# Optimization experiments

Measured on AMD Instinct MI355X. Metric: run time of the kernel, lower is better.

The kernel has to match this reference:

```python
import jax, jax.numpy as jnp
import numpy as np

TEMPERATURE = 0.05


def setup_inputs() -> dict:
    key = jax.random.key(0)
    k1, k2 = jax.random.split(key)
    B, D = 4096, 1024
    # scale 0.1 keeps pairwise distances O(3) so the original exp(-d/T) is sane
    text_embeddings = 0.1 * jax.random.normal(k1, (B, D), dtype=jnp.float32)
    image_embeddings = 0.1 * jax.random.normal(k2, (B, D), dtype=jnp.float32)
    positive_pairs = jnp.arange(B, dtype=jnp.int32)  # unused by the loss body
    return {
        "text_embeddings": text_embeddings,
        "image_embeddings": image_embeddings,
        "positive_pairs": positive_pairs,
    }


def _pairwise_l2(t, m):
    # ||t_i - m_j|| via GEMM expansion; [B, B]
    sq = (
        jnp.sum(t * t, axis=1, keepdims=True)
        + jnp.sum(m * m, axis=1)[None, :]
        - 2.0 * (t @ m.T)
    )
    return jnp.sqrt(jnp.maximum(sq, 0.0))


def reference(text_embeddings, image_embeddings, positive_pairs):
    # loss_i = -log( exp(-d_ii/T) / sum_{j != i} exp(-d_ij/T) )
    #        = logsumexp_{j != i}(-d_ij/T) + d_ii/T   (exact same math, stable)
    dist = _pairwise_l2(text_embeddings, image_embeddings)  # [B, B]
    logits = -dist / TEMPERATURE
    diag = jnp.diagonal(logits)  # log numerator per row
    B = logits.shape[0]
    eye = jnp.eye(B, dtype=bool)
    masked = jnp.where(eye, -jnp.inf, logits)  # exclude self-term from denom
    lse = jax.nn.logsumexp(masked, axis=1)
    return jnp.mean(lse - diag)
```

## Files before the change

kernel.cpp:

```cpp
#include <hip/hip_runtime.h>
#include <math.h>


#define NB 4096
#define ND 1024
#define LSE_BIAS 90.0f
#define A2 28.85390082f
#define C2 129.8425537f
#define LN2 0.6931471805599453f
#define SCALE1 0x7F7F7F7Fu

typedef int v8i __attribute__((ext_vector_type(8)));
typedef int int4v __attribute__((ext_vector_type(4)));
typedef float v16f __attribute__((ext_vector_type(16)));

__device__ inline void gload_lds16(const unsigned char* g, unsigned char* l) {
  __builtin_amdgcn_global_load_lds(
      (const __attribute__((address_space(1))) unsigned int*)g,
      (__attribute__((address_space(3))) unsigned int*)l, 16, 0, 0);
}

__global__ void prep_kernel(const float* __restrict__ T, const float* __restrict__ M,
                            unsigned char* __restrict__ t8, unsigned char* __restrict__ m8,
                            float* __restrict__ tn, float* __restrict__ mn,
                            float* __restrict__ out) {
  int row = blockIdx.x;
  if (row == 0 && threadIdx.x == 0) out[0] = 0.0f;
  const float* src;
  unsigned char* dst;
  float* nout;
  int r;
  if (row < NB) { src = T; dst = t8; nout = tn; r = row; }
  else          { src = M; dst = m8; nout = mn; r = row - NB; }
  float4 v = ((const float4*)(src + (size_t)r * ND))[threadIdx.x];
  float s = v.x * v.x + v.y * v.y + v.z * v.z + v.w * v.w;
  int p = __builtin_amdgcn_cvt_pk_fp8_f32(v.x, v.y, 0, false);
  p = __builtin_amdgcn_cvt_pk_fp8_f32(v.z, v.w, p, true);
  ((int*)(dst + (size_t)r * ND))[threadIdx.x] = p;
  for (int off = 32; off; off >>= 1) s += __shfl_xor(s, off);
  __shared__ float wsum[4];
  if ((threadIdx.x & 63) == 0) wsum[threadIdx.x >> 6] = s;
  __syncthreads();
  if (threadIdx.x == 0) nout[r] = wsum[0] + wsum[1] + wsum[2] + wsum[3];
}

__launch_bounds__(256, 3)
__global__ void gemm_lse_kernel(const unsigned char* __restrict__ t8,
                                const unsigned char* __restrict__ m8,
                                const float* __restrict__ tn, const float* __restrict__ mn,
                                float* __restrict__ part_s, float* __restrict__ diag) {
  __shared__ unsigned char Al[128 * 128];
  __shared__ unsigned char Bl[128 * 128];
  int rt = blockIdx.x, ct = blockIdx.y;
  int tid = threadIdx.x;
  int wave = tid >> 6, lane = tid & 63;
  int hb = lane >> 5, l31 = lane & 31;

  v16f acc[2][2] = {};

  int l3 = lane >> 3;
  int gc = (lane & 7) ^ l3;
  const unsigned char* gA = t8 + (size_t)(rt * 128 + wave * 32 + l3) * ND + gc * 16;
  const unsigned char* gB = m8 + (size_t)(ct * 128 + wave * 32 + l3) * ND + gc * 16;
  unsigned char* lA = Al + wave * 4096;
  unsigned char* lB = Bl + wave * 4096;

  int wr0 = (wave >> 1) * 64, wc0 = (wave & 1) * 64;
  int sw = l31 & 7;
  int abase = (wr0 + l31) * 128;
  int bbase = (wc0 + l31) * 128;

#pragma unroll 1
  for (int kt = 0; kt < ND / 128; ++kt) {
#pragma unroll
    for (int i = 0; i < 4; ++i) {
      gload_lds16(gA + (size_t)i * 8 * ND, lA + i * 1024);
      gload_lds16(gB + (size_t)i * 8 * ND, lB + i * 1024);
    }
    __syncthreads();
#pragma unroll
    for (int ks = 0; ks < 2; ++ks) {
      int q16 = ((ks * 4 + 2 * hb) ^ sw) * 16;
      int4v a00 = *(const int4v*)&Al[abase + q16];
      int4v a01 = *(const int4v*)&Al[abase + (q16 ^ 16)];
      int4v a10 = *(const int4v*)&Al[abase + 4096 + q16];
      int4v a11 = *(const int4v*)&Al[abase + 4096 + (q16 ^ 16)];
      v8i af0 = (v8i){a00.x, a00.y, a00.z, a00.w, a01.x, a01.y, a01.z, a01.w};
      v8i af1 = (v8i){a10.x, a10.y, a10.z, a10.w, a11.x, a11.y, a11.z, a11.w};
#pragma unroll
      for (int fc = 0; fc < 2; ++fc) {
        int4v b0 = *(const int4v*)&Bl[bbase + fc * 4096 + q16];
        int4v b1 = *(const int4v*)&Bl[bbase + fc * 4096 + (q16 ^ 16)];
        v8i bf = (v8i){b0.x, b0.y, b0.z, b0.w, b1.x, b1.y, b1.z, b1.w};
        acc[0][fc] = __builtin_amdgcn_mfma_scale_f32_32x32x64_f8f6f4(
            af0, bf, acc[0][fc], 0, 0, 0, SCALE1, 0, SCALE1);
        acc[1][fc] = __builtin_amdgcn_mfma_scale_f32_32x32x64_f8f6f4(
            af1, bf, acc[1][fc], 0, 0, 0, SCALE1, 0, SCALE1);
      }
    }
    __syncthreads();
    gA += 128;
    gB += 128;
  }

  int chunk = ct * 2 + (wave & 1);
  bool diagblk = (rt == ct);
  float mnv[2];
#pragma unroll
  for (int fc = 0; fc < 2; ++fc) mnv[fc] = mn[ct * 128 + wc0 + fc * 32 + l31];
#pragma unroll
  for (int fr = 0; fr < 2; ++fr) {
#pragma unroll
    for (int reg = 0; reg < 16; ++reg) {
      int row = (reg & 3) + 8 * (reg >> 2) + 4 * hb;
      int grow = rt * 128 + wr0 + fr * 32 + row;
      float tnr = tn[grow];
      float s = 0.0f;
#pragma unroll
      for (int fc = 0; fc < 2; ++fc) {
        float sq = fmaxf(fmaf(-2.0f, acc[fr][fc][reg], tnr + mnv[fc]), 0.0f);
        float dr = __builtin_amdgcn_sqrtf(sq);
        float e = __builtin_amdgcn_exp2f(fmaf(dr, -A2, C2));
        if (diagblk) {
          int gcol = ct * 128 + wc0 + fc * 32 + l31;
          if (grow == gcol) {
            diag[grow] = -20.0f * dr;
            e = 0.0f;
          }
        }
        s += e;
      }
      for (int m = 16; m; m >>= 1) s += __shfl_xor(s, m);
      if (l31 == 0) part_s[(size_t)grow * 64 + chunk] = s;
    }
  }
}

__global__ void combine_kernel(const float* __restrict__ part_s,
                               const float* __restrict__ diag, float* __restrict__ out) {
  int row = blockIdx.x * 256 + threadIdx.x;
  const float* ps = part_s + (size_t)row * 64;
  float S = 0.0f;
#pragma unroll 8
  for (int c = 0; c < 64; ++c) S += ps[c];
  float loss = (LN2 * __builtin_amdgcn_logf(S) - LSE_BIAS) - diag[row];
  for (int off = 32; off; off >>= 1) loss += __shfl_xor(loss, off);
  __shared__ float wsum[4];
  if ((threadIdx.x & 63) == 0) wsum[threadIdx.x >> 6] = loss;
  __syncthreads();
  if (threadIdx.x == 0)
    atomicAdd(out, (wsum[0] + wsum[1] + wsum[2] + wsum[3]) * (1.0f / (float)NB));
}

extern "C" void kernel_launch(void* const* d_in, const int* in_sizes, int n_in,
                              void* d_out, int out_size, void* d_ws, size_t ws_size,
                              hipStream_t stream) {
  const float* T = (const float*)d_in[0];
  const float* M = (const float*)d_in[1];
  float* out = (float*)d_out;

  unsigned char* t8 = (unsigned char*)d_ws;
  unsigned char* m8 = t8 + (size_t)NB * ND;
  float* fbase = (float*)(m8 + (size_t)NB * ND);
  float* tn = fbase;
  float* mn = tn + NB;
  float* diag = mn + NB;
  float* part_s = diag + NB;

  prep_kernel<<<2 * NB, 256, 0, stream>>>(T, M, t8, m8, tn, mn, out);
  dim3 grid(NB / 128, NB / 128);
  gemm_lse_kernel<<<grid, 256, 0, stream>>>(t8, m8, tn, mn, part_s, diag);
  combine_kernel<<<NB / 256, 256, 0, stream>>>(part_s, diag, out);
}
```

Measured before the change: 107.5 us.

## Use 256x256 tiles with double-buffered LDS staging and grouped block order

The fused GEMM+LSE kernel now computes a 256x256 output tile per 512-thread block instead of 128x128 per 256-thread block. Each wave now holds four row fragments, which raises operand reuse per LDS read. The kernel ping-pongs two LDS buffers, issuing the next K-slice's global-to-LDS loads before computing the current slice so load latency overlaps the MFMAs. It also remaps block indices into grouped regions for L2 locality and raises wave priority around the MFMA section. The cost is 128KB of LDS per block and more accumulator registers, so only one block fits per CU, and the 256-block grid roughly matches the CU count.

```diff
diff --git a/kernel.cpp b/kernel.cpp
--- a/kernel.cpp
+++ b/kernel.cpp
@@ -44,76 +44,92 @@
   if (threadIdx.x == 0) nout[r] = wsum[0] + wsum[1] + wsum[2] + wsum[3];
 }
 
-__launch_bounds__(256, 3)
+__launch_bounds__(512, 2)
 __global__ void gemm_lse_kernel(const unsigned char* __restrict__ t8,
                                 const unsigned char* __restrict__ m8,
                                 const float* __restrict__ tn, const float* __restrict__ mn,
                                 float* __restrict__ part_s, float* __restrict__ diag) {
-  __shared__ unsigned char Al[128 * 128];
-  __shared__ unsigned char Bl[128 * 128];
-  int rt = blockIdx.x, ct = blockIdx.y;
+  __shared__ unsigned char A0[256 * 128];
+  __shared__ unsigned char A1[256 * 128];
+  __shared__ unsigned char B0[256 * 128];
+  __shared__ unsigned char B1[256 * 128];
+  int b = blockIdx.x;
+  int region = b & 7, idx = b >> 3;
+  int rt = ((region >> 2) << 3) | (idx & 7);
+  int ct = ((region & 3) << 2) | (idx >> 3);
   int tid = threadIdx.x;
   int wave = tid >> 6, lane = tid & 63;
   int hb = lane >> 5, l31 = lane & 31;
+  int wr = wave >> 2, wc = wave & 3;
 
-  v16f acc[2][2] = {};
+  v16f acc[4][2] = {};
 
   int l3 = lane >> 3;
   int gc = (lane & 7) ^ l3;
-  const unsigned char* gA = t8 + (size_t)(rt * 128 + wave * 32 + l3) * ND + gc * 16;
-  const unsigned char* gB = m8 + (size_t)(ct * 128 + wave * 32 + l3) * ND + gc * 16;
-  unsigned char* lA = Al + wave * 4096;
-  unsigned char* lB = Bl + wave * 4096;
+  const unsigned char* gA = t8 + (size_t)(rt * 256 + wave * 32 + l3) * ND + gc * 16;
+  const unsigned char* gB = m8 + (size_t)(ct * 256 + wave * 32 + l3) * ND + gc * 16;
 
-  int wr0 = (wave >> 1) * 64, wc0 = (wave & 1) * 64;
   int sw = l31 & 7;
-  int abase = (wr0 + l31) * 128;
-  int bbase = (wc0 + l31) * 128;
+  int arow = (wr * 128 + l31) * 128;
+  int brow = (wc * 64 + l31) * 128;
+
+#define STAGE(DA, DB, koff)                                                  \
+  do {                                                                       \
+    _Pragma("unroll") for (int i = 0; i < 4; ++i) {                          \
+      gload_lds16(gA + (koff) + (size_t)i * 8 * ND, DA + wave * 4096 + i * 1024); \
+      gload_lds16(gB + (koff) + (size_t)i * 8 * ND, DB + wave * 4096 + i * 1024); \
+    }                                                                        \
+  } while (0)
+
+#define COMPUTE(SA, SB)                                                      \
+  do {                                                                       \
+    _Pragma("unroll") for (int ks = 0; ks < 2; ++ks) {                       \
+      int q16 = ((ks * 4 + 2 * hb) ^ sw) * 16;                               \
+      v8i af[4];                                                             \
+      _Pragma("unroll") for (int fr = 0; fr < 4; ++fr) {                     \
+        int4v x0 = *(const int4v*)&SA[arow + fr * 4096 + q16];               \
+        int4v x1 = *(const int4v*)&SA[arow + fr * 4096 + (q16 ^ 16)];        \
+        af[fr] = (v8i){x0.x, x0.y, x0.z, x0.w, x1.x, x1.y, x1.z, x1.w};      \
+      }                                                                      \
+      __builtin_amdgcn_s_setprio(1);                                         \
+      _Pragma("unroll") for (int fc = 0; fc < 2; ++fc) {                     \
+        int4v y0 = *(const int4v*)&SB[brow + fc * 4096 + q16];               \
+        int4v y1 = *(const int4v*)&SB[brow + fc * 4096 + (q16 ^ 16)];        \
+        v8i bf = (v8i){y0.x, y0.y, y0.z, y0.w, y1.x, y1.y, y1.z, y1.w};      \
+        _Pragma("unroll") for (int fr = 0; fr < 4; ++fr)                     \
+          acc[fr][fc] = __builtin_amdgcn_mfma_scale_f32_32x32x64_f8f6f4(     \
+              af[fr], bf, acc[fr][fc], 0, 0, 0, SCALE1, 0, SCALE1);          \
+      }                                                                      \
+      __builtin_amdgcn_s_setprio(0);                                         \
+    }                                                                        \
+  } while (0)
+
+  STAGE(A0, B0, 0);
+  __syncthreads();
 
 #pragma unroll 1
-  for (int kt = 0; kt < ND / 128; ++kt) {
-#pragma unroll
-    for (int i = 0; i < 4; ++i) {
-      gload_lds16(gA + (size_t)i * 8 * ND, lA + i * 1024);
-      gload_lds16(gB + (size_t)i * 8 * ND, lB + i * 1024);
-    }
+  for (int kt2 = 0; kt2 < 4; ++kt2) {
+    STAGE(A1, B1, (kt2 * 2 + 1) * 128);
+    COMPUTE(A0, B0);
     __syncthreads();
-#pragma unroll
-    for (int ks = 0; ks < 2; ++ks) {
-      int q16 = ((ks * 4 + 2 * hb) ^ sw) * 16;
-      int4v a00 = *(const int4v*)&Al[abase + q16];
-      int4v a01 = *(const int4v*)&Al[abase + (q16 ^ 16)];
-      int4v a10 = *(const int4v*)&Al[abase + 4096 + q16];
-      int4v a11 = *(const int4v*)&Al[abase + 4096 + (q16 ^ 16)];
-      v8i af0 = (v8i){a00.x, a00.y, a00.z, a00.w, a01.x, a01.y, a01.z, a01.w};
-      v8i af1 = (v8i){a10.x, a10.y, a10.z, a10.w, a11.x, a11.y, a11.z, a11.w};
-#pragma unroll
-      for (int fc = 0; fc < 2; ++fc) {
-        int4v b0 = *(const int4v*)&Bl[bbase + fc * 4096 + q16];
-        int4v b1 = *(const int4v*)&Bl[bbase + fc * 4096 + (q16 ^ 16)];
-        v8i bf = (v8i){b0.x, b0.y, b0.z, b0.w, b1.x, b1.y, b1.z, b1.w};
-        acc[0][fc] = __builtin_amdgcn_mfma_scale_f32_32x32x64_f8f6f4(
-            af0, bf, acc[0][fc], 0, 0, 0, SCALE1, 0, SCALE1);
-        acc[1][fc] = __builtin_amdgcn_mfma_scale_f32_32x32x64_f8f6f4(
-            af1, bf, acc[1][fc], 0, 0, 0, SCALE1, 0, SCALE1);
-      }
-    }
+    if (kt2 < 3) STAGE(A0, B0, (kt2 * 2 + 2) * 128);
+    COMPUTE(A1, B1);
     __syncthreads();
-    gA += 128;
-    gB += 128;
   }
+#undef STAGE
+#undef COMPUTE
 
-  int chunk = ct * 2 + (wave & 1);
+  int chunk = ct * 4 + wc;
   bool diagblk = (rt == ct);
   float mnv[2];
 #pragma unroll
-  for (int fc = 0; fc < 2; ++fc) mnv[fc] = mn[ct * 128 + wc0 + fc * 32 + l31];
+  for (int fc = 0; fc < 2; ++fc) mnv[fc] = mn[ct * 256 + wc * 64 + fc * 32 + l31];
 #pragma unroll
-  for (int fr = 0; fr < 2; ++fr) {
+  for (int fr = 0; fr < 4; ++fr) {
 #pragma unroll
     for (int reg = 0; reg < 16; ++reg) {
       int row = (reg & 3) + 8 * (reg >> 2) + 4 * hb;
-      int grow = rt * 128 + wr0 + fr * 32 + row;
+      int grow = rt * 256 + wr * 128 + fr * 32 + row;
       float tnr = tn[grow];
       float s = 0.0f;
 #pragma unroll
@@ -122,7 +138,7 @@
         float dr = __builtin_amdgcn_sqrtf(sq);
         float e = __builtin_amdgcn_exp2f(fmaf(dr, -A2, C2));
         if (diagblk) {
-          int gcol = ct * 128 + wc0 + fc * 32 + l31;
+          int gcol = ct * 256 + wc * 64 + fc * 32 + l31;
           if (grow == gcol) {
             diag[grow] = -20.0f * dr;
             e = 0.0f;
@@ -168,7 +184,6 @@
   float* part_s = diag + NB;
 
   prep_kernel<<<2 * NB, 256, 0, stream>>>(T, M, t8, m8, tn, mn, out);
-  dim3 grid(NB / 128, NB / 128);
-  gemm_lse_kernel<<<grid, 256, 0, stream>>>(t8, m8, tn, mn, part_s, diag);
+  gemm_lse_kernel<<<(NB / 256) * (NB / 256), 512, 0, stream>>>(t8, m8, tn, mn, part_s, diag);
   combine_kernel<<<NB / 256, 256, 0, stream>>>(part_s, diag, out);
 }
```

New measurement: 121.7 us. +13.2%, slower.
